# Kernel tuning notes

Hardware: AMD Instinct MI355X
Metric: run time of the kernel (lower is better)

The kernel has to match this reference:

```python
import jax, jax.numpy as jnp
import numpy as np

B, H, W, C = 64, 224, 224, 3
P = 16
DIM = 768
DEPTH = 12
NH, DH = 12, 64
FF = 3072
NPATCH = (H // P) * (W // P)   # 196
L = NPATCH + 1                 # 197 tokens (CLS + patches)
KEEP = int(L * (1.0 - 0.75))   # 49 unmasked tokens


def setup_inputs() -> dict:
    key = jax.random.key(0)
    ks = jax.random.split(key, 16)
    s = 0.02
    inp = {
        'inputs': jax.random.normal(ks[0], (B, H, W, C), jnp.float32),
        'conv_w': jax.random.normal(ks[1], (P, P, C, DIM), jnp.float32) * s,
        'ct':     jax.random.normal(ks[2], (1, 1, DIM), jnp.float32) * s,
        'pe':     jax.random.normal(ks[3], (1, L, DIM), jnp.float32) * s,
        'ln1_s': jnp.ones((DEPTH, DIM), jnp.float32),
        'ln1_b': jnp.zeros((DEPTH, DIM), jnp.float32),
        'qkv_w': jax.random.normal(ks[4], (DEPTH, DIM, 3 * NH * DH), jnp.float32) * s,
        'proj_w': jax.random.normal(ks[5], (DEPTH, NH * DH, DIM), jnp.float32) * s,
        'ln2_s': jnp.ones((DEPTH, DIM), jnp.float32),
        'ln2_b': jnp.zeros((DEPTH, DIM), jnp.float32),
        'w1': jax.random.normal(ks[6], (DEPTH, DIM, FF), jnp.float32) * s,
        'b1': jnp.zeros((DEPTH, FF), jnp.float32),
        'w2': jax.random.normal(ks[7], (DEPTH, FF, DIM), jnp.float32) * s,
        'b2': jnp.zeros((DEPTH, DIM), jnp.float32),
        # Faithful to original: permutation of arange(1, L+1); max value 197
        # is out-of-range and gets clamped by JAX gather, exactly as upstream.
        'mask_idx': jax.random.permutation(ks[8], jnp.arange(1, L + 1))[:KEEP].astype(jnp.int32),
    }
    return inp


def _layernorm(x, scale, bias, eps=1e-9):
    m = jnp.mean(x, axis=-1, keepdims=True)
    v = jnp.var(x, axis=-1, keepdims=True)
    return (x - m) * jax.lax.rsqrt(v + eps) * scale + bias


def _encoder(x, layer_params):
    # x: [B, KEEP, DIM]; layer_params leaves stacked on axis 0 (DEPTH)
    inv_sqrt_d = 1.0 / jnp.sqrt(jnp.float32(DH))

    def block(x, p):
        ln1s, ln1b, qw, pw, ln2s, ln2b, w1, b1, w2, b2 = p
        h = _layernorm(x, ln1s, ln1b)
        qkv = h @ qw                                   # [B, Lk, 3*NH*DH]
        q, k, v = jnp.split(qkv, 3, axis=-1)
        def heads(t):
            return t.reshape(x.shape[0], -1, NH, DH).transpose(0, 2, 1, 3)
        q, k, v = heads(q), heads(k), heads(v)         # [B, NH, Lk, DH]
        att = jax.nn.softmax(jnp.einsum('bhqd,bhkd->bhqk', q, k) * inv_sqrt_d)
        o = jnp.einsum('bhqk,bhkd->bhqd', att, v)
        o = o.transpose(0, 2, 1, 3).reshape(x.shape[0], -1, NH * DH) @ pw
        x = x + o
        h2 = _layernorm(x, ln2s, ln2b)
        x = x + (jax.nn.gelu(h2 @ w1 + b1) @ w2 + b2)
        return x, None

    x, _ = jax.lax.scan(block, x, layer_params)
    return x


def reference(inputs, conv_w, ct, pe, ln1_s, ln1_b, qkv_w, proj_w,
              ln2_s, ln2_b, w1, b1, w2, b2, mask_idx):
    # patch embed: stride-P conv, no bias
    out = jax.lax.conv_general_dilated(
        inputs, conv_w, window_strides=(P, P), padding='VALID',
        dimension_numbers=('NHWC', 'HWIO', 'NHWC'))      # [B, 14, 14, DIM]
    out = out.reshape(out.shape[0], -1, out.shape[3])     # [B, 196, DIM]
    out = jnp.concatenate((jnp.repeat(ct, out.shape[0], axis=0), out), axis=1)
    out = out + pe                                        # [B, 197, DIM]
    patches = out[:, mask_idx]                            # [B, 49, DIM]
    layer_params = (ln1_s, ln1_b, qkv_w, proj_w, ln2_s, ln2_b, w1, b1, w2, b2)
    return _encoder(patches, layer_params)
```

## Files before the change

### kernel.cpp

```cpp
#include <hip/hip_runtime.h>
#include <hip/hip_bf16.h>
#include <math.h>

#define DIMV   768
#define BATCH  64
#define KEEPT  49
#define MTOK   (BATCH*KEEPT)
#define NHEADS 12
#define DHEAD  64
#define FFV    3072
#define NDEPTH 12

typedef short short8 __attribute__((ext_vector_type(8)));
typedef float floatx4 __attribute__((ext_vector_type(4)));
typedef unsigned short ushort;

__device__ __forceinline__ void async_cp16(const void* g, void* l) {
  __builtin_amdgcn_global_load_lds((const __attribute__((address_space(1))) void*)g,
                                   (__attribute__((address_space(3))) void*)l,
                                   16, 0, 0);
}

__global__ __launch_bounds__(256) void gather_patches(
    const float* __restrict__ inp, const int* __restrict__ mask,
    __hip_bfloat16* __restrict__ apix)
{
  int gid = blockIdx.x * 256 + threadIdx.x;
  if (gid >= MTOK * DIMV) return;
  int r = gid / DIMV, k = gid - r * DIMV;
  int b = r / KEEPT, t = r - b * KEEPT;
  int j = mask[t];
  j = j < 0 ? 0 : (j > 196 ? 196 : j);
  float v = 0.f;
  if (j > 0) {
    int p  = j - 1, py = p / 14, px = p - py * 14;
    int ky = k / 48, rem = k - ky * 48, kx = rem / 3, c = rem - kx * 3;
    v = inp[(((b * 224) + py * 16 + ky) * 224 + px * 16 + kx) * 3 + c];
  }
  apix[gid] = __float2bfloat16(v);
}

__global__ __launch_bounds__(256) void finish_embed(
    float* __restrict__ x, const float* __restrict__ ct,
    const float* __restrict__ pe, const int* __restrict__ mask)
{
  int gid = blockIdx.x * 256 + threadIdx.x;
  if (gid >= MTOK * DIMV) return;
  int r = gid / DIMV, d = gid - r * DIMV;
  int t = r % KEEPT;
  int j = mask[t];
  j = j < 0 ? 0 : (j > 196 ? 196 : j);
  float base = (j == 0) ? ct[d] : x[gid];
  x[gid] = base + pe[j * DIMV + d];
}

__global__ __launch_bounds__(256) void layernorm_k(
    const float* __restrict__ x, const float* __restrict__ sc,
    const float* __restrict__ bi, __hip_bfloat16* __restrict__ out)
{
  __shared__ float red[8];
  int r = blockIdx.x;
  const float* xr = x + (size_t)r * DIMV;
  int t = threadIdx.x;
  float v[3];
  float s = 0.f, ss = 0.f;
#pragma unroll
  for (int i = 0; i < 3; i++) {
    float a = xr[t + i * 256];
    v[i] = a; s += a; ss += a * a;
  }
#pragma unroll
  for (int off = 32; off > 0; off >>= 1) {
    s  += __shfl_down(s,  off, 64);
    ss += __shfl_down(ss, off, 64);
  }
  int wave = t >> 6, lane = t & 63;
  if (lane == 0) { red[wave] = s; red[4 + wave] = ss; }
  __syncthreads();
  if (t == 0) {
    float a  = red[0] + red[1] + red[2] + red[3];
    float b2 = red[4] + red[5] + red[6] + red[7];
    float m  = a * (1.f / DIMV);
    float var = b2 * (1.f / DIMV) - m * m;
    red[0] = m;
    red[1] = rsqrtf(var + 1e-9f);
  }
  __syncthreads();
  float m = red[0], rs = red[1];
  __hip_bfloat16* outr = out + (size_t)r * DIMV;
#pragma unroll
  for (int i = 0; i < 3; i++) {
    int d = t + i * 256;
    outr[d] = __float2bfloat16((v[i] - m) * rs * sc[d] + bi[d]);
  }
}

__device__ __forceinline__ void transpose_tile(
    const float* __restrict__ src, __hip_bfloat16* __restrict__ dst,
    int R, int C, int tr, int tcc)
{
  __shared__ float lds[32][33];
  int x = threadIdx.x & 31, y = threadIdx.x >> 5;
  int r0 = tr * 32, c0 = tcc * 32;
#pragma unroll
  for (int i = 0; i < 4; i++)
    lds[y + 8 * i][x] = src[(size_t)(r0 + y + 8 * i) * C + c0 + x];
  __syncthreads();
#pragma unroll
  for (int i = 0; i < 4; i++)
    dst[(size_t)(c0 + y + 8 * i) * R + r0 + x] = __float2bfloat16(lds[x][y + 8 * i]);
}

__global__ __launch_bounds__(256) void transpose_one(
    const float* __restrict__ src, __hip_bfloat16* __restrict__ dst, int R, int C)
{
  int tc = C >> 5;
  transpose_tile(src, dst, R, C, blockIdx.x / tc, blockIdx.x % tc);
}

#define QKV_TE  ((size_t)2304*768)
#define PROJ_TE ((size_t)768*768)
#define W1_TE   ((size_t)3072*768)
#define W2_TE   ((size_t)768*3072)
#define LSTRIDE (QKV_TE + PROJ_TE + W1_TE + W2_TE)

__global__ __launch_bounds__(256) void convert_weights(
    const float* __restrict__ qkv_w, const float* __restrict__ proj_w,
    const float* __restrict__ w1, const float* __restrict__ w2,
    __hip_bfloat16* __restrict__ dstBase, int layer0, size_t dstStride)
{
  int l = layer0 + blockIdx.y;
  __hip_bfloat16* d = dstBase + (size_t)blockIdx.y * dstStride;
  int tile = blockIdx.x;
  const float* src; __hip_bfloat16* dst; int R, C, t0;
  if (tile < 1728)      { src = qkv_w  + (size_t)l*768*2304; dst = d;                          R=768;  C=2304; t0=tile; }
  else if (tile < 2304) { src = proj_w + (size_t)l*768*768;  dst = d + QKV_TE;                 R=768;  C=768;  t0=tile-1728; }
  else if (tile < 4608) { src = w1     + (size_t)l*768*3072; dst = d + QKV_TE+PROJ_TE;         R=768;  C=3072; t0=tile-2304; }
  else                  { src = w2     + (size_t)l*3072*768; dst = d + QKV_TE+PROJ_TE+W1_TE;   R=3072; C=768;  t0=tile-4608; }
  int tc = C >> 5;
  transpose_tile(src, dst, R, C, t0 / tc, t0 % tc);
}

enum { EPI_NONE = 0, EPI_RESID = 1, EPI_BIAS_GELU = 2, EPI_BIAS_RESID = 3 };

template <int TN, int EPI, bool OUT_BF16>
__global__ __launch_bounds__(256) void gemm_mfma(
    const ushort* __restrict__ A, const ushort* __restrict__ Bt,
    const float* __restrict__ Cin, const float* __restrict__ bias,
    void* __restrict__ Cout, int M, int N, int K)
{
  constexpr int AM = (TN == 128) ? 4 : 2;
  constexpr int B_LOADS = TN / 64;
  __shared__ ushort As[128 * 32];
  __shared__ ushort Bs[TN * 32];

  const int tid  = threadIdx.x;
  const int wave = tid >> 6, lane = tid & 63;
  const int bm = blockIdx.y, bn = blockIdx.x;

  const int wm0 = (TN == 128) ? (wave & 1) * 64 : wave * 32;
  const int wn0 = (TN == 128) ? (wave >> 1) * 64 : 0;

  floatx4 acc[AM][4];
#pragma unroll
  for (int i = 0; i < AM; i++)
#pragma unroll
    for (int j = 0; j < 4; j++) { floatx4 z = {0.f,0.f,0.f,0.f}; acc[i][j] = z; }

  const int lrow = lane >> 2, lchunk = (lane & 3) * 8;
  const ushort* aSrc[2];
  ushort*       aDst[2];
#pragma unroll
  for (int i = 0; i < 2; i++) {
    int row = bm * 128 + (wave * 2 + i) * 16 + lrow;
    row = row < M - 1 ? row : M - 1;
    aSrc[i] = A + (size_t)row * K + lchunk;
    aDst[i] = As + (wave * 2 + i) * 512;
  }
  const ushort* bSrc[B_LOADS];
  ushort*       bDst[B_LOADS];
#pragma unroll
  for (int i = 0; i < B_LOADS; i++) {
    int row = bn * TN + (wave * B_LOADS + i) * 16 + lrow;
    bSrc[i] = Bt + (size_t)row * K + lchunk;
    bDst[i] = Bs + (wave * B_LOADS + i) * 512;
  }

  for (int k0 = 0; k0 < K; k0 += 32) {
    __syncthreads();
#pragma unroll
    for (int i = 0; i < 2; i++)       async_cp16(aSrc[i] + k0, aDst[i]);
#pragma unroll
    for (int i = 0; i < B_LOADS; i++) async_cp16(bSrc[i] + k0, bDst[i]);
    __syncthreads();

    short8 af[AM], bf[4];
#pragma unroll
    for (int mt = 0; mt < AM; mt++)
      af[mt] = *(const short8*)&As[(wm0 + mt * 16 + (lane & 15)) * 32 + (lane >> 4) * 8];
#pragma unroll
    for (int nt = 0; nt < 4; nt++)
      bf[nt] = *(const short8*)&Bs[(wn0 + nt * 16 + (lane & 15)) * 32 + (lane >> 4) * 8];
#pragma unroll
    for (int mt = 0; mt < AM; mt++)
#pragma unroll
      for (int nt = 0; nt < 4; nt++)
        acc[mt][nt] = __builtin_amdgcn_mfma_f32_16x16x32_bf16(af[mt], bf[nt], acc[mt][nt], 0, 0, 0);
  }

  const int colb = bn * TN + wn0 + (lane & 15);
  const int rq   = (lane >> 4) * 4;
#pragma unroll
  for (int mt = 0; mt < AM; mt++) {
#pragma unroll
    for (int r = 0; r < 4; r++) {
      int row = bm * 128 + wm0 + mt * 16 + rq + r;
      if (row >= M) continue;
#pragma unroll
      for (int nt = 0; nt < 4; nt++) {
        int col = colb + nt * 16;
        float u = acc[mt][nt][r];
        if (EPI == EPI_BIAS_GELU || EPI == EPI_BIAS_RESID) u += bias[col];
        if (EPI == EPI_BIAS_GELU) {
          float t3 = u * u * u;
          u = 0.5f * u * (1.f + tanhf(0.7978845608028654f * (u + 0.044715f * t3)));
        }
        if (EPI == EPI_RESID || EPI == EPI_BIAS_RESID) u += Cin[(size_t)row * N + col];
        if (OUT_BF16)
          ((__hip_bfloat16*)Cout)[(size_t)row * N + col] = __float2bfloat16(u);
        else
          ((float*)Cout)[(size_t)row * N + col] = u;
      }
    }
  }
}

__global__ __launch_bounds__(64) void attn_k(
    const __hip_bfloat16* __restrict__ qkv, __hip_bfloat16* __restrict__ o)
{
  __shared__ float qs[49][65];
  __shared__ float ks[49][64];
  __shared__ float vs[49][64];
  __shared__ float ssc[49][50];
  int b = blockIdx.x, hh = blockIdx.y;
  int t = threadIdx.x;

  for (int idx = t; idx < 49 * 64; idx += 64) {
    int tok = idx >> 6, d = idx & 63;
    size_t base = (size_t)(b * KEEPT + tok) * (3 * DIMV) + hh * 64 + d;
    qs[tok][d] = __bfloat162float(qkv[base]);
    ks[tok][d] = __bfloat162float(qkv[base + DIMV]);
    vs[tok][d] = __bfloat162float(qkv[base + 2 * DIMV]);
  }
  __syncthreads();

  if (t < KEEPT) {
    float mx = -1e30f;
    for (int j = 0; j < KEEPT; j++) {
      float acc = 0.f;
#pragma unroll
      for (int d = 0; d < 64; d++) acc += qs[t][d] * ks[j][d];
      acc *= 0.125f;
      ssc[t][j] = acc;
      mx = fmaxf(mx, acc);
    }
    float sum = 0.f;
    for (int j = 0; j < KEEPT; j++) {
      float e = __expf(ssc[t][j] - mx);
      ssc[t][j] = e;
      sum += e;
    }
    float inv = 1.f / sum;
    float oa[64];
#pragma unroll
    for (int d = 0; d < 64; d++) oa[d] = 0.f;
    for (int j = 0; j < KEEPT; j++) {
      float w = ssc[t][j] * inv;
#pragma unroll
      for (int d = 0; d < 64; d++) oa[d] += w * vs[j][d];
    }
    __hip_bfloat16* orow = o + (size_t)(b * KEEPT + t) * DIMV + hh * 64;
#pragma unroll
    for (int d = 0; d < 64; d++) orow[d] = __float2bfloat16(oa[d]);
  }
}

extern "C" void kernel_launch(void* const* d_in, const int* in_sizes, int n_in,
                              void* d_out, int out_size, void* d_ws, size_t ws_size,
                              hipStream_t stream)
{
  (void)in_sizes; (void)n_in; (void)out_size;
  const float* inputs = (const float*)d_in[0];
  const float* conv_w = (const float*)d_in[1];
  const float* ct     = (const float*)d_in[2];
  const float* pe     = (const float*)d_in[3];
  const float* ln1_s  = (const float*)d_in[4];
  const float* ln1_b  = (const float*)d_in[5];
  const float* qkv_w  = (const float*)d_in[6];
  const float* proj_w = (const float*)d_in[7];
  const float* ln2_s  = (const float*)d_in[8];
  const float* ln2_b  = (const float*)d_in[9];
  const float* w1     = (const float*)d_in[10];
  const float* b1     = (const float*)d_in[11];
  const float* w2     = (const float*)d_in[12];
  const float* b2     = (const float*)d_in[13];
  const int*   mask   = (const int*)d_in[14];
  float* out = (float*)d_out;

  char* wsb = (char*)d_ws;
  float*          x     = (float*)wsb;
  __hip_bfloat16* h     = (__hip_bfloat16*)(wsb + 9633792);
  __hip_bfloat16* big   = (__hip_bfloat16*)(wsb + 9633792 + 4816896);
  __hip_bfloat16* convT = (__hip_bfloat16*)(wsb + 9633792 + 4816896 + 19267584);
  __hip_bfloat16* wbuf  = (__hip_bfloat16*)(wsb + 9633792 + 4816896 + 19267584 + 1179648);
  const size_t base_bytes = 9633792ull + 4816896 + 19267584 + 1179648;
  const bool all_mode = ws_size >= base_bytes + 12ull * LSTRIDE * 2;

  __hip_bfloat16* apix = h;
  __hip_bfloat16* qkv  = big;
  __hip_bfloat16* g    = big;

  dim3 blk(256);
  const int nelem = MTOK * DIMV;
  const int nblk  = (nelem + 255) / 256;
  const int mg    = (MTOK + 127) / 128;

  transpose_one<<<576, blk, 0, stream>>>(conv_w, convT, 768, 768);
  if (all_mode)
    convert_weights<<<dim3(6912, 12), blk, 0, stream>>>(
        qkv_w, proj_w, w1, w2, wbuf, 0, LSTRIDE);

  gather_patches<<<nblk, blk, 0, stream>>>(inputs, mask, apix);
  gemm_mfma<64, EPI_NONE, false><<<dim3(12, mg), blk, 0, stream>>>(
      (const ushort*)apix, (const ushort*)convT, nullptr, nullptr, x,
      MTOK, DIMV, DIMV);
  finish_embed<<<nblk, blk, 0, stream>>>(x, ct, pe, mask);

  for (int l = 0; l < NDEPTH; l++) {
    __hip_bfloat16* wl = wbuf + (all_mode ? (size_t)l * LSTRIDE : 0);
    if (!all_mode)
      convert_weights<<<dim3(6912, 1), blk, 0, stream>>>(
          qkv_w, proj_w, w1, w2, wbuf, l, 0);
    const ushort* qkvT  = (const ushort*)wl;
    const ushort* projT = (const ushort*)(wl + QKV_TE);
    const ushort* w1T   = (const ushort*)(wl + QKV_TE + PROJ_TE);
    const ushort* w2T   = (const ushort*)(wl + QKV_TE + PROJ_TE + W1_TE);

    layernorm_k<<<MTOK, blk, 0, stream>>>(x, ln1_s + l * DIMV, ln1_b + l * DIMV, h);
    gemm_mfma<128, EPI_NONE, true><<<dim3(18, mg), blk, 0, stream>>>(
        (const ushort*)h, qkvT, nullptr, nullptr, qkv, MTOK, 3 * DIMV, DIMV);
    attn_k<<<dim3(BATCH, NHEADS), dim3(64), 0, stream>>>(qkv, h);
    gemm_mfma<64, EPI_RESID, false><<<dim3(12, mg), blk, 0, stream>>>(
        (const ushort*)h, projT, x, nullptr, x, MTOK, DIMV, DIMV);
    layernorm_k<<<MTOK, blk, 0, stream>>>(x, ln2_s + l * DIMV, ln2_b + l * DIMV, h);
    gemm_mfma<128, EPI_BIAS_GELU, true><<<dim3(24, mg), blk, 0, stream>>>(
        (const ushort*)h, w1T, nullptr, b1 + (size_t)l * FFV, g, MTOK, FFV, DIMV);
    float* dst = (l == NDEPTH - 1) ? out : x;
    gemm_mfma<64, EPI_BIAS_RESID, false><<<dim3(12, mg), blk, 0, stream>>>(
        (const ushort*)g, w2T, x, b2 + (size_t)l * DIMV, dst, MTOK, DIMV, FFV);
  }
}
```

Before: 2.730 ms.

## Use MFMA for attention and widen weight transpose tiles to 64x64

```diff
diff --git a/kernel.cpp b/kernel.cpp
--- a/kernel.cpp
+++ b/kernel.cpp
@@ -14,6 +14,11 @@
 typedef short short8 __attribute__((ext_vector_type(8)));
 typedef float floatx4 __attribute__((ext_vector_type(4)));
 typedef unsigned short ushort;
+
+__device__ __forceinline__ ushort f2bf(float f) {
+  __hip_bfloat16 h = __float2bfloat16(f);
+  return *(ushort*)&h;
+}
 
 __device__ __forceinline__ void async_cp16(const void* g, void* l) {
   __builtin_amdgcn_global_load_lds((const __attribute__((address_space(1))) void*)g,
@@ -95,27 +100,41 @@
   }
 }
 
-__device__ __forceinline__ void transpose_tile(
+__device__ __forceinline__ void transpose_tile64(
     const float* __restrict__ src, __hip_bfloat16* __restrict__ dst,
     int R, int C, int tr, int tcc)
 {
-  __shared__ float lds[32][33];
-  int x = threadIdx.x & 31, y = threadIdx.x >> 5;
-  int r0 = tr * 32, c0 = tcc * 32;
-#pragma unroll
-  for (int i = 0; i < 4; i++)
-    lds[y + 8 * i][x] = src[(size_t)(r0 + y + 8 * i) * C + c0 + x];
+  __shared__ float lds[64][65];
+  const int tid = threadIdx.x;
+  const int r0 = tr * 64, c0 = tcc * 64;
+  const int lr = tid >> 4, lc4 = (tid & 15) * 4;
+#pragma unroll
+  for (int p = 0; p < 4; p++) {
+    float4 v = *(const float4*)(src + (size_t)(r0 + p * 16 + lr) * C + c0 + lc4);
+    lds[p * 16 + lr][lc4 + 0] = v.x;
+    lds[p * 16 + lr][lc4 + 1] = v.y;
+    lds[p * 16 + lr][lc4 + 2] = v.z;
+    lds[p * 16 + lr][lc4 + 3] = v.w;
+  }
   __syncthreads();
 #pragma unroll
-  for (int i = 0; i < 4; i++)
-    dst[(size_t)(c0 + y + 8 * i) * R + r0 + x] = __float2bfloat16(lds[x][y + 8 * i]);
+  for (int p = 0; p < 4; p++) {
+    int c  = p * 16 + (tid >> 4);
+    int rc = (tid & 15) * 4;
+    ushort4 ov;
+    ov.x = f2bf(lds[rc + 0][c]);
+    ov.y = f2bf(lds[rc + 1][c]);
+    ov.z = f2bf(lds[rc + 2][c]);
+    ov.w = f2bf(lds[rc + 3][c]);
+    *(ushort4*)((ushort*)dst + (size_t)(c0 + c) * R + r0 + rc) = ov;
+  }
 }
 
 __global__ __launch_bounds__(256) void transpose_one(
     const float* __restrict__ src, __hip_bfloat16* __restrict__ dst, int R, int C)
 {
-  int tc = C >> 5;
-  transpose_tile(src, dst, R, C, blockIdx.x / tc, blockIdx.x % tc);
+  int tc = C >> 6;
+  transpose_tile64(src, dst, R, C, blockIdx.x / tc, blockIdx.x % tc);
 }
 
 #define QKV_TE  ((size_t)2304*768)
@@ -133,12 +152,12 @@
   __hip_bfloat16* d = dstBase + (size_t)blockIdx.y * dstStride;
   int tile = blockIdx.x;
   const float* src; __hip_bfloat16* dst; int R, C, t0;
-  if (tile < 1728)      { src = qkv_w  + (size_t)l*768*2304; dst = d;                          R=768;  C=2304; t0=tile; }
-  else if (tile < 2304) { src = proj_w + (size_t)l*768*768;  dst = d + QKV_TE;                 R=768;  C=768;  t0=tile-1728; }
-  else if (tile < 4608) { src = w1     + (size_t)l*768*3072; dst = d + QKV_TE+PROJ_TE;         R=768;  C=3072; t0=tile-2304; }
-  else                  { src = w2     + (size_t)l*3072*768; dst = d + QKV_TE+PROJ_TE+W1_TE;   R=3072; C=768;  t0=tile-4608; }
-  int tc = C >> 5;
-  transpose_tile(src, dst, R, C, t0 / tc, t0 % tc);
+  if (tile < 432)       { src = qkv_w  + (size_t)l*768*2304; dst = d;                          R=768;  C=2304; t0=tile; }
+  else if (tile < 576)  { src = proj_w + (size_t)l*768*768;  dst = d + QKV_TE;                 R=768;  C=768;  t0=tile-432; }
+  else if (tile < 1152) { src = w1     + (size_t)l*768*3072; dst = d + QKV_TE+PROJ_TE;         R=768;  C=3072; t0=tile-576; }
+  else                  { src = w2     + (size_t)l*3072*768; dst = d + QKV_TE+PROJ_TE+W1_TE;   R=3072; C=768;  t0=tile-1152; }
+  int tc = C >> 6;
+  transpose_tile64(src, dst, R, C, t0 / tc, t0 % tc);
 }
 
 enum { EPI_NONE = 0, EPI_RESID = 1, EPI_BIAS_GELU = 2, EPI_BIAS_RESID = 3 };
@@ -235,54 +254,127 @@
   }
 }
 
-__global__ __launch_bounds__(64) void attn_k(
-    const __hip_bfloat16* __restrict__ qkv, __hip_bfloat16* __restrict__ o)
-{
-  __shared__ float qs[49][65];
-  __shared__ float ks[49][64];
-  __shared__ float vs[49][64];
-  __shared__ float ssc[49][50];
-  int b = blockIdx.x, hh = blockIdx.y;
-  int t = threadIdx.x;
-
-  for (int idx = t; idx < 49 * 64; idx += 64) {
-    int tok = idx >> 6, d = idx & 63;
-    size_t base = (size_t)(b * KEEPT + tok) * (3 * DIMV) + hh * 64 + d;
-    qs[tok][d] = __bfloat162float(qkv[base]);
-    ks[tok][d] = __bfloat162float(qkv[base + DIMV]);
-    vs[tok][d] = __bfloat162float(qkv[base + 2 * DIMV]);
+__global__ __launch_bounds__(64) void attn_mfma(
+    const ushort* __restrict__ qkv, ushort* __restrict__ o)
+{
+  __shared__ ushort qA[64 * 72];
+  __shared__ ushort kB[64 * 72];
+  __shared__ ushort vT[64 * 72];
+  __shared__ ushort pA[64 * 72];
+  const int b = blockIdx.x, hh = blockIdx.y;
+  const int lane = threadIdx.x;
+  const int fr = lane & 15, fc = lane >> 4;
+
+  const ushort* base = qkv + (size_t)b * KEEPT * (3 * DIMV) + hh * 64;
+  for (int r = 0; r < KEEPT; r++) {
+    const ushort* row = base + (size_t)r * (3 * DIMV);
+    qA[r * 72 + lane] = row[lane];
+    kB[r * 72 + lane] = row[DIMV + lane];
+    vT[lane * 72 + r] = row[2 * DIMV + lane];
+  }
+#pragma unroll
+  for (int r = KEEPT; r < 64; r++) {
+    qA[r * 72 + lane] = 0;
+    kB[r * 72 + lane] = 0;
+    vT[lane * 72 + r] = 0;
   }
   __syncthreads();
 
-  if (t < KEEPT) {
-    float mx = -1e30f;
-    for (int j = 0; j < KEEPT; j++) {
-      float acc = 0.f;
-#pragma unroll
-      for (int d = 0; d < 64; d++) acc += qs[t][d] * ks[j][d];
-      acc *= 0.125f;
-      ssc[t][j] = acc;
-      mx = fmaxf(mx, acc);
+  floatx4 sacc[4][4];
+#pragma unroll
+  for (int mt = 0; mt < 4; mt++)
+#pragma unroll
+    for (int nt = 0; nt < 4; nt++) { floatx4 z = {0.f,0.f,0.f,0.f}; sacc[mt][nt] = z; }
+
+#pragma unroll
+  for (int kk = 0; kk < 2; kk++) {
+    const int ch = kk * 32 + fc * 8;
+    short8 af[4], bf[4];
+#pragma unroll
+    for (int mt = 0; mt < 4; mt++) af[mt] = *(const short8*)&qA[(mt * 16 + fr) * 72 + ch];
+#pragma unroll
+    for (int nt = 0; nt < 4; nt++) bf[nt] = *(const short8*)&kB[(nt * 16 + fr) * 72 + ch];
+#pragma unroll
+    for (int mt = 0; mt < 4; mt++)
+#pragma unroll
+      for (int nt = 0; nt < 4; nt++)
+        sacc[mt][nt] = __builtin_amdgcn_mfma_f32_16x16x32_bf16(af[mt], bf[nt], sacc[mt][nt], 0, 0, 0);
+  }
+
+  float inv[4][4];
+#pragma unroll
+  for (int mt = 0; mt < 4; mt++) {
+#pragma unroll
+    for (int r = 0; r < 4; r++) {
+      float mx = -1e30f;
+#pragma unroll
+      for (int nt = 0; nt < 4; nt++) {
+        float s = sacc[mt][nt][r] * 0.125f;
+        if (nt == 3 && fr >= 1) s = -1e30f;
+        sacc[mt][nt][r] = s;
+        mx = fmaxf(mx, s);
+      }
+      mx = fmaxf(mx, __shfl_xor(mx, 1, 64));
+      mx = fmaxf(mx, __shfl_xor(mx, 2, 64));
+      mx = fmaxf(mx, __shfl_xor(mx, 4, 64));
+      mx = fmaxf(mx, __shfl_xor(mx, 8, 64));
+      float sum = 0.f;
+#pragma unroll
+      for (int nt = 0; nt < 4; nt++) {
+        float e = __expf(sacc[mt][nt][r] - mx);
+        sacc[mt][nt][r] = e;
+        sum += e;
+      }
+      sum += __shfl_xor(sum, 1, 64);
+      sum += __shfl_xor(sum, 2, 64);
+      sum += __shfl_xor(sum, 4, 64);
+      sum += __shfl_xor(sum, 8, 64);
+      inv[mt][r] = 1.f / sum;
     }
-    float sum = 0.f;
-    for (int j = 0; j < KEEPT; j++) {
-      float e = __expf(ssc[t][j] - mx);
-      ssc[t][j] = e;
-      sum += e;
+  }
+
+#pragma unroll
+  for (int mt = 0; mt < 4; mt++)
+#pragma unroll
+    for (int r = 0; r < 4; r++)
+#pragma unroll
+      for (int nt = 0; nt < 4; nt++)
+        pA[(mt * 16 + fc * 4 + r) * 72 + nt * 16 + fr] = f2bf(sacc[mt][nt][r]);
+  __syncthreads();
+
+  floatx4 oacc[4][4];
+#pragma unroll
+  for (int mt = 0; mt < 4; mt++)
+#pragma unroll
+    for (int nt = 0; nt < 4; nt++) { floatx4 z = {0.f,0.f,0.f,0.f}; oacc[mt][nt] = z; }
+
+#pragma unroll
+  for (int kk = 0; kk < 2; kk++) {
+    const int ch = kk * 32 + fc * 8;
+    short8 af[4], bf[4];
+#pragma unroll
+    for (int mt = 0; mt < 4; mt++) af[mt] = *(const short8*)&pA[(mt * 16 + fr) * 72 + ch];
+#pragma unroll
+    for (int nt = 0; nt < 4; nt++) bf[nt] = *(const short8*)&vT[(nt * 16 + fr) * 72 + ch];
+#pragma unroll
+    for (int mt = 0; mt < 4; mt++)
+#pragma unroll
+      for (int nt = 0; nt < 4; nt++)
+        oacc[mt][nt] = __builtin_amdgcn_mfma_f32_16x16x32_bf16(af[mt], bf[nt], oacc[mt][nt], 0, 0, 0);
+  }
+
+  ushort* obase = o + (size_t)b * KEEPT * DIMV + hh * 64;
+#pragma unroll
+  for (int mt = 0; mt < 4; mt++)
+#pragma unroll
+    for (int r = 0; r < 4; r++) {
+      int q = mt * 16 + fc * 4 + r;
+      if (q < KEEPT) {
+#pragma unroll
+        for (int nt = 0; nt < 4; nt++)
+          obase[(size_t)q * DIMV + nt * 16 + fr] = f2bf(oacc[mt][nt][r] * inv[mt][r]);
+      }
     }
-    float inv = 1.f / sum;
-    float oa[64];
-#pragma unroll
-    for (int d = 0; d < 64; d++) oa[d] = 0.f;
-    for (int j = 0; j < KEEPT; j++) {
-      float w = ssc[t][j] * inv;
-#pragma unroll
-      for (int d = 0; d < 64; d++) oa[d] += w * vs[j][d];
-    }
-    __hip_bfloat16* orow = o + (size_t)(b * KEEPT + t) * DIMV + hh * 64;
-#pragma unroll
-    for (int d = 0; d < 64; d++) orow[d] = __float2bfloat16(oa[d]);
-  }
 }
 
 extern "C" void kernel_launch(void* const* d_in, const int* in_sizes, int n_in,
@@ -325,9 +417,9 @@
   const int nblk  = (nelem + 255) / 256;
   const int mg    = (MTOK + 127) / 128;
 
-  transpose_one<<<576, blk, 0, stream>>>(conv_w, convT, 768, 768);
+  transpose_one<<<144, blk, 0, stream>>>(conv_w, convT, 768, 768);
   if (all_mode)
-    convert_weights<<<dim3(6912, 12), blk, 0, stream>>>(
+    convert_weights<<<dim3(1728, 12), blk, 0, stream>>>(
         qkv_w, proj_w, w1, w2, wbuf, 0, LSTRIDE);
 
   gather_patches<<<nblk, blk, 0, stream>>>(inputs, mask, apix);
@@ -339,7 +431,7 @@
   for (int l = 0; l < NDEPTH; l++) {
     __hip_bfloat16* wl = wbuf + (all_mode ? (size_t)l * LSTRIDE : 0);
     if (!all_mode)
-      convert_weights<<<dim3(6912, 1), blk, 0, stream>>>(
+      convert_weights<<<dim3(1728, 1), blk, 0, stream>>>(
           qkv_w, proj_w, w1, w2, wbuf, l, 0);
     const ushort* qkvT  = (const ushort*)wl;
     const ushort* projT = (const ushort*)(wl + QKV_TE);
@@ -349,7 +441,8 @@
     layernorm_k<<<MTOK, blk, 0, stream>>>(x, ln1_s + l * DIMV, ln1_b + l * DIMV, h);
     gemm_mfma<128, EPI_NONE, true><<<dim3(18, mg), blk, 0, stream>>>(
         (const ushort*)h, qkvT, nullptr, nullptr, qkv, MTOK, 3 * DIMV, DIMV);
-    attn_k<<<dim3(BATCH, NHEADS), dim3(64), 0, stream>>>(qkv, h);
+    attn_mfma<<<dim3(BATCH, NHEADS), dim3(64), 0, stream>>>(
+        (const ushort*)qkv, (ushort*)h);
     gemm_mfma<64, EPI_RESID, false><<<dim3(12, mg), blk, 0, stream>>>(
         (const ushort*)h, projT, x, nullptr, x, MTOK, DIMV, DIMV);
     layernorm_k<<<MTOK, blk, 0, stream>>>(x, ln2_s + l * DIMV, ln2_b + l * DIMV, h);
```

Result: faster. 2.500 ms (-8.4%).
